# Kernel tuning notes

Measured on AMD Instinct MI355X. Metric: run time of the kernel, lower is better.

The kernel has to match this reference:

```python
import jax, jax.numpy as jnp
import numpy as np

N = 50000      # nodes
E = 800000     # edges (avg degree 16)
D_IN = 128     # input_dim
H = 64         # hidden_dim (== output_dim)
L = 3          # num_layers


def setup_inputs() -> dict:
    key = jax.random.key(0)
    ks = jax.random.split(key, 24)
    s = 0.05
    p = lambda k, shape: jax.random.normal(k, shape, dtype=jnp.float32) * s
    inp = {}
    inp["node_features"] = jax.random.normal(ks[0], (N, D_IN), dtype=jnp.float32)
    inp["edge_index"] = jax.random.randint(ks[1], (2, E), 0, N, dtype=jnp.int32)
    # pre_mlp: Linear-ReLU-Linear (setup_LRL_nn with hidden_sizes=[hidden_dim])
    inp["pre_w1"] = p(ks[2], (D_IN, H)); inp["pre_b1"] = jnp.zeros((H,), jnp.float32)
    inp["pre_w2"] = p(ks[3], (H, H));    inp["pre_b2"] = jnp.zeros((H,), jnp.float32)
    # learnable skip gates (initialized to ones as in the module)
    inp["skip"] = jnp.ones((L, L), jnp.float32)
    # SAGEConv layers: lin_l (on mean-aggregated neighbors, with bias) + lin_r (root)
    for i in range(L):
        din = H * (i + 1)
        inp[f"wl{i}"] = p(ks[4 + 3 * i], (din, H))
        inp[f"bl{i}"] = jnp.zeros((H,), jnp.float32)
        inp[f"wr{i}"] = p(ks[5 + 3 * i], (din, H))
    # post_mlp: 256->64, 64->64, 64->256, 256->64
    inp["post_w1"] = p(ks[14], (H * (L + 1), H)); inp["post_b1"] = jnp.zeros((H,), jnp.float32)
    inp["post_w2"] = p(ks[15], (H, H));           inp["post_b2"] = jnp.zeros((H,), jnp.float32)
    inp["post_w3"] = p(ks[16], (H, 256));         inp["post_b3"] = jnp.zeros((256,), jnp.float32)
    inp["post_w4"] = p(ks[17], (256, H));         inp["post_b4"] = jnp.zeros((H,), jnp.float32)
    return inp


def _sage(x, src, dst, inv_deg, wl, bl, wr):
    # PyG SAGEConv (mean aggr): lin_l(mean_{j->i} x_j) + lin_r(x_i)
    agg = jax.ops.segment_sum(x[src], dst, num_segments=N) * inv_deg  # [N, Din]
    return agg @ wl + bl + x @ wr


def reference(node_features, edge_index,
              pre_w1, pre_b1, pre_w2, pre_b2, skip,
              wl0, bl0, wr0, wl1, bl1, wr1, wl2, bl2, wr2,
              post_w1, post_b1, post_w2, post_b2, post_w3, post_b3, post_w4, post_b4):
    src, dst = edge_index[0], edge_index[1]
    deg = jax.ops.segment_sum(jnp.ones((E,), jnp.float32), dst, num_segments=N)
    inv_deg = (1.0 / jnp.maximum(deg, 1.0))[:, None]  # [N,1]

    # pre_mlp
    x = jax.nn.relu(node_features @ pre_w1 + pre_b1) @ pre_w2 + pre_b2  # [N,H]

    layers = [(wl0, bl0, wr0), (wl1, bl1, wr1), (wl2, bl2, wr2)]
    all_emb = [x]
    emb = x
    for i, (wl, bl, wr) in enumerate(layers):
        gates = jax.nn.sigmoid(skip[i, :i + 1])  # [i+1]
        curr = jnp.concatenate([all_emb[j] * gates[j] for j in range(i + 1)], axis=1)  # [N, H*(i+1)]
        h = jax.nn.relu(_sage(curr, src, dst, inv_deg, wl, bl, wr))  # [N,H]  (dropout p=0)
        emb = jnp.concatenate([emb, h], axis=1)
        all_emb.append(h)

    s = jnp.sum(emb, axis=-2)  # sums over all nodes -> [H*(L+1)] (faithful to source)
    h = jax.nn.leaky_relu(s @ post_w1 + post_b1, negative_slope=0.1)
    h = jax.nn.relu(h @ post_w2 + post_b2)
    h = jax.nn.relu(h @ post_w3 + post_b3)
    return h @ post_w4 + post_b4  # [H]
```

## Files before the change

### kernel.cpp

```cpp
#include <hip/hip_runtime.h>
#include <math.h>

#define NN 50000
#define NE 800000
#define NB 196

typedef float v4f __attribute__((ext_vector_type(4)));
typedef short v8s __attribute__((ext_vector_type(8)));

__device__ __forceinline__ unsigned short f2bf(float f) {
  unsigned u = __float_as_uint(f);
  u = u + 0x7FFFu + ((u >> 16) & 1u);
  return (unsigned short)(u >> 16);
}
__device__ __forceinline__ float bf2f(unsigned short h) {
  return __uint_as_float(((unsigned)h) << 16);
}


__global__ __launch_bounds__(256) void k_bhist(const int* __restrict__ dst,
                                               int* __restrict__ gbcnt) {
  __shared__ int lcnt[NB];
  int t = threadIdx.x;
  for (int i = t; i < NB; i += 256) lcnt[i] = 0;
  __syncthreads();
  int eb = blockIdx.x * 4096;
#pragma unroll
  for (int i = 0; i < 16; ++i) {
    int e = eb + i * 256 + t;
    if (e < NE) atomicAdd(&lcnt[dst[e] >> 8], 1);
  }
  __syncthreads();
  for (int i = t; i < NB; i += 256)
    if (lcnt[i]) atomicAdd(&gbcnt[i], lcnt[i]);
}

__global__ __launch_bounds__(256) void k_bscan(const int* __restrict__ gbcnt,
                                               int* __restrict__ boff,
                                               int* __restrict__ gcur,
                                               int* __restrict__ offs) {
  __shared__ int sd[256];
  int t = threadIdx.x;
  int v = (t < NB) ? gbcnt[t] : 0;
  sd[t] = v;
  __syncthreads();
  for (int o = 1; o < 256; o <<= 1) {
    int u = (t >= o) ? sd[t - o] : 0;
    __syncthreads();
    sd[t] += u;
    __syncthreads();
  }
  if (t < NB) { int x = sd[t] - v; boff[t] = x; gcur[t] = x; }
  if (t == NB - 1) boff[NB] = sd[t];
  if (t == 0) offs[NN] = NE;
}

__global__ __launch_bounds__(256) void k_bscatter(const int* __restrict__ src,
                                                  const int* __restrict__ dst,
                                                  int* __restrict__ gcur,
                                                  unsigned* __restrict__ ebuf) {
  __shared__ int cnt[NB];
  __shared__ int base[NB];
  int t = threadIdx.x;
  for (int i = t; i < NB; i += 256) cnt[i] = 0;
  __syncthreads();
  int eb = blockIdx.x * 4096;
  unsigned pk[16];
  int bk[16], lp[16];
#pragma unroll
  for (int i = 0; i < 16; ++i) {
    int e = eb + i * 256 + t;
    if (e < NE) {
      int d = dst[e];
      int b = d >> 8;
      pk[i] = ((unsigned)src[e] << 8) | (unsigned)(d & 255);
      bk[i] = b;
      lp[i] = atomicAdd(&cnt[b], 1);
    }
  }
  __syncthreads();
  for (int i = t; i < NB; i += 256)
    base[i] = cnt[i] ? atomicAdd(&gcur[i], cnt[i]) : 0;
  __syncthreads();
#pragma unroll
  for (int i = 0; i < 16; ++i) {
    int e = eb + i * 256 + t;
    if (e < NE) ebuf[base[bk[i]] + lp[i]] = pk[i];
  }
}

__global__ __launch_bounds__(256) void k_bbuild(const unsigned* __restrict__ ebuf,
                                                const int* __restrict__ boff,
                                                int* __restrict__ offs,
                                                float* __restrict__ invd,
                                                int* __restrict__ csr) {
  __shared__ int dcnt[256];
  __shared__ int cur[256];
  int t = threadIdx.x;
  int b = blockIdx.x;
  int node0 = b << 8;
  int es = boff[b], ee = boff[b + 1];
  dcnt[t] = 0;
  __syncthreads();
  for (int e = es + t; e < ee; e += 256) atomicAdd(&dcnt[ebuf[e] & 255], 1);
  __syncthreads();
  int v = dcnt[t];
  cur[t] = v;
  __syncthreads();
  for (int o = 1; o < 256; o <<= 1) {
    int u = (t >= o) ? cur[t - o] : 0;
    __syncthreads();
    cur[t] += u;
    __syncthreads();
  }
  int excl = cur[t] - v;
  int node = node0 + t;
  if (node < NN) {
    offs[node] = es + excl;
    invd[node] = 1.0f / fmaxf((float)v, 1.0f);
  }
  __syncthreads();
  cur[t] = es + excl;
  __syncthreads();
  for (int e = es + t; e < ee; e += 256) {
    unsigned pk = ebuf[e];
    int p = atomicAdd(&cur[pk & 255], 1);
    csr[p] = (int)(pk >> 8);
  }
}

__global__ __launch_bounds__(256) void k_aggregate(
    const unsigned short* __restrict__ feat,
    const int* __restrict__ offs, const int* __restrict__ csr,
    const float* __restrict__ invd,
    unsigned short* __restrict__ mean, int n) {
  int node = blockIdx.x * 4 + (threadIdx.x >> 6);
  int lane = threadIdx.x & 63;
  int nsub = lane >> 4;
  int cg   = lane & 15;
  if (node >= n) return;
  int s = offs[node], e = offs[node + 1];

  float a[8];
#pragma unroll
  for (int i = 0; i < 8; ++i) a[i] = 0.f;

  if (e > s) {
    int emax = e - 1;
    for (int p0 = s; p0 < e; p0 += 16) {
      int pa = p0 + nsub, pb = p0 + 4 + nsub, pc = p0 + 8 + nsub, pd = p0 + 12 + nsub;
      int ja = csr[pa < emax ? pa : emax];
      int jb = csr[pb < emax ? pb : emax];
      int jc = csr[pc < emax ? pc : emax];
      int jd = csr[pd < emax ? pd : emax];
      v8s va = *(const v8s*)(feat + (size_t)ja * 128 + cg * 8);
      v8s vb = *(const v8s*)(feat + (size_t)jb * 128 + cg * 8);
      v8s vc = *(const v8s*)(feat + (size_t)jc * 128 + cg * 8);
      v8s vd = *(const v8s*)(feat + (size_t)jd * 128 + cg * 8);
      if (pa < e) {
#pragma unroll
        for (int i = 0; i < 8; ++i) a[i] += bf2f((unsigned short)va[i]);
      }
      if (pb < e) {
#pragma unroll
        for (int i = 0; i < 8; ++i) a[i] += bf2f((unsigned short)vb[i]);
      }
      if (pc < e) {
#pragma unroll
        for (int i = 0; i < 8; ++i) a[i] += bf2f((unsigned short)vc[i]);
      }
      if (pd < e) {
#pragma unroll
        for (int i = 0; i < 8; ++i) a[i] += bf2f((unsigned short)vd[i]);
      }
    }
  }
#pragma unroll
  for (int i = 0; i < 8; ++i) {
    a[i] += __shfl_xor(a[i], 8, 64);
    a[i] += __shfl_xor(a[i], 16, 64);
    a[i] += __shfl_xor(a[i], 32, 64);
  }
  if (lane < 8) {
    float d = invd[node];
    v8s oh, ol;
#pragma unroll
    for (int i = 0; i < 8; ++i) {
      float m = a[i] * d;
      unsigned short h = f2bf(m);
      oh[i] = (short)h;
      ol[i] = (short)f2bf(m - bf2f(h));
    }
    *(v8s*)(mean + (size_t)node * 128 + lane * 8) = oh;
    *(v8s*)(mean + (size_t)node * 128 + 64 + lane * 8) = ol;
  }
}

struct WPrepArgs {
  const float* w[15];
  int gidx[15];
  const float* skip;
  unsigned short* wbuf;
};

__global__ __launch_bounds__(256) void k_wprep(WPrepArgs P) {
  int slot = blockIdx.x;
  int t = threadIdx.x;
  const float* w = P.w[slot];
  float gs = 1.0f;
  if (P.gidx[slot] >= 0) gs = 1.0f / (1.0f + __expf(-P.skip[P.gidx[slot]]));
  unsigned short* hi = P.wbuf + (size_t)slot * 8192;
  unsigned short* lo = hi + 4096;
#pragma unroll
  for (int half = 0; half < 2; ++half) {
    int p = t + 256 * half;
    int frag = p >> 6, lane = p & 63;
    int ks = frag >> 2, ct = frag & 3;
    int qd = lane >> 4, ln = lane & 15;
    v8s hv, lv;
#pragma unroll
    for (int j = 0; j < 8; ++j) {
      float f = w[(size_t)(ks * 32 + qd * 8 + j) * 64 + ct * 16 + ln] * gs;
      unsigned short h = f2bf(f);
      hv[j] = (short)h;
      lv[j] = (short)f2bf(f - bf2f(h));
    }
    *(v8s*)(hi + (size_t)p * 8) = hv;
    *(v8s*)(lo + (size_t)p * 8) = lv;
  }
}

struct LinArgs {
  const void* a[6];
  int isf32[6];
  int stride[6];
  int slot0;
  int nsrc;
  const float* bias;
  const unsigned short* wbuf;
  unsigned short* outp;
  float* colsum;
  int n;
  int relu;
};

__global__ __launch_bounds__(256) void k_linear(LinArgs A) {
  __shared__ float red[256];
  const int t    = threadIdx.x;
  const int lane = t & 63;
  const int wv   = t >> 6;
  const int qd   = lane >> 4;
  const int ln   = lane & 15;
  const int n0   = blockIdx.x * 64;

  v4f acc[4];
#pragma unroll
  for (int ct = 0; ct < 4; ++ct) acc[ct] = (v4f){0.f, 0.f, 0.f, 0.f};

  const int arow = n0 + wv * 16 + ln;
  const bool arv = arow < A.n;

  v8s rawh[2], rawl[2];
  float rawf[16];
  v8s curh[2], curl[2];
  auto loadA = [&](int s) {
    if (A.isf32[s]) {
      const float* a = (const float*)A.a[s];
      int st = A.stride[s];
      if (arv) {
#pragma unroll
        for (int ks = 0; ks < 2; ++ks) {
          const float* p = a + (size_t)arow * st + ks * 32 + qd * 8;
          float4 u0 = *(const float4*)(p);
          float4 u1 = *(const float4*)(p + 4);
          rawf[ks * 8 + 0] = u0.x; rawf[ks * 8 + 1] = u0.y;
          rawf[ks * 8 + 2] = u0.z; rawf[ks * 8 + 3] = u0.w;
          rawf[ks * 8 + 4] = u1.x; rawf[ks * 8 + 5] = u1.y;
          rawf[ks * 8 + 6] = u1.z; rawf[ks * 8 + 7] = u1.w;
        }
      } else {
#pragma unroll
        for (int j = 0; j < 16; ++j) rawf[j] = 0.f;
      }
    } else {
      const unsigned short* ph = (const unsigned short*)A.a[s] + (size_t)arow * 128;
      if (arv) {
#pragma unroll
        for (int ks = 0; ks < 2; ++ks) {
          rawh[ks] = *(const v8s*)(ph + ks * 32 + qd * 8);
          rawl[ks] = *(const v8s*)(ph + 64 + ks * 32 + qd * 8);
        }
      } else {
        v8s z;
#pragma unroll
        for (int j = 0; j < 8; ++j) z[j] = 0;
        rawh[0] = rawh[1] = rawl[0] = rawl[1] = z;
      }
    }
  };
  auto stageA = [&](int s) {
    if (A.isf32[s]) {
#pragma unroll
      for (int ks = 0; ks < 2; ++ks) {
        v8s hv, lv;
#pragma unroll
        for (int j = 0; j < 8; ++j) {
          float f = rawf[ks * 8 + j];
          unsigned short h = f2bf(f);
          hv[j] = (short)h;
          lv[j] = (short)f2bf(f - bf2f(h));
        }
        curh[ks] = hv; curl[ks] = lv;
      }
    } else {
#pragma unroll
      for (int ks = 0; ks < 2; ++ks) { curh[ks] = rawh[ks]; curl[ks] = rawl[ks]; }
    }
  };

  loadA(0);
  stageA(0);

  for (int s = 0; s < A.nsrc; ++s) {
    if (s + 1 < A.nsrc) loadA(s + 1);
    const unsigned short* wb = A.wbuf + (size_t)(A.slot0 + s) * 8192;
#pragma unroll
    for (int ks = 0; ks < 2; ++ks) {
#pragma unroll
      for (int ct = 0; ct < 4; ++ct) {
        const unsigned short* fp = wb + (size_t)((ks * 4 + ct) * 64 + lane) * 8;
        v8s bh = *(const v8s*)(fp);
        v8s bl = *(const v8s*)(fp + 4096);
        acc[ct] = __builtin_amdgcn_mfma_f32_16x16x32_bf16(curh[ks], bh, acc[ct], 0, 0, 0);
        acc[ct] = __builtin_amdgcn_mfma_f32_16x16x32_bf16(curl[ks], bh, acc[ct], 0, 0, 0);
        acc[ct] = __builtin_amdgcn_mfma_f32_16x16x32_bf16(curh[ks], bl, acc[ct], 0, 0, 0);
      }
    }
    if (s + 1 < A.nsrc) stageA(s + 1);
  }

  float bvals[4];
#pragma unroll
  for (int ct = 0; ct < 4; ++ct) bvals[ct] = A.bias[ct * 16 + ln];

  float cs[4] = {0.f, 0.f, 0.f, 0.f};
#pragma unroll
  for (int ct = 0; ct < 4; ++ct) {
#pragma unroll
    for (int r = 0; r < 4; ++r) {
      int node = n0 + wv * 16 + qd * 4 + r;
      float v = acc[ct][r] + bvals[ct];
      if (A.relu) v = fmaxf(v, 0.f);
      if (node < A.n) {
        unsigned short h = f2bf(v);
        A.outp[(size_t)node * 128 + ct * 16 + ln] = h;
        A.outp[(size_t)node * 128 + 64 + ct * 16 + ln] = f2bf(v - bf2f(h));
        cs[ct] += v;
      }
    }
  }
  if (A.colsum) {
#pragma unroll
    for (int ct = 0; ct < 4; ++ct) {
      float v = cs[ct];
      v += __shfl_xor(v, 16, 64);
      v += __shfl_xor(v, 32, 64);
      if (qd == 0) red[wv * 64 + ct * 16 + ln] = v;
    }
    __syncthreads();
    if (t < 64) {
      float ssum = red[t] + red[64 + t] + red[128 + t] + red[192 + t];
      atomicAdd(&A.colsum[t], ssum);
    }
  }
}

__global__ __launch_bounds__(256) void k_post(const float* __restrict__ s,
                                              const float* __restrict__ w1, const float* __restrict__ b1,
                                              const float* __restrict__ w2, const float* __restrict__ b2,
                                              const float* __restrict__ w3, const float* __restrict__ b3,
                                              const float* __restrict__ w4, const float* __restrict__ b4,
                                              float* __restrict__ outp) {
  __shared__ float sh[256], h1[64], h2[64], h3[256];
  int t = threadIdx.x;
  sh[t] = s[t];
  __syncthreads();
  if (t < 64) {
    float a = b1[t];
    for (int k = 0; k < 256; ++k) a += sh[k] * w1[k * 64 + t];
    h1[t] = (a >= 0.f) ? a : 0.1f * a;
  }
  __syncthreads();
  if (t < 64) {
    float a = b2[t];
    for (int k = 0; k < 64; ++k) a += h1[k] * w2[k * 64 + t];
    h2[t] = fmaxf(a, 0.f);
  }
  __syncthreads();
  {
    float a = b3[t];
    for (int k = 0; k < 64; ++k) a += h2[k] * w3[k * 256 + t];
    h3[t] = fmaxf(a, 0.f);
  }
  __syncthreads();
  if (t < 64) {
    float a = b4[t];
    for (int k = 0; k < 256; ++k) a += h3[k] * w4[k * 64 + t];
    outp[t] = a;
  }
}

extern "C" void kernel_launch(void* const* d_in, const int* in_sizes, int n_in,
                              void* d_out, int out_size, void* d_ws, size_t ws_size,
                              hipStream_t stream) {
  const float* nf     = (const float*)d_in[0];
  const int*   ei     = (const int*)d_in[1];
  const float* pre_w1 = (const float*)d_in[2];
  const float* pre_b1 = (const float*)d_in[3];
  const float* pre_w2 = (const float*)d_in[4];
  const float* pre_b2 = (const float*)d_in[5];
  const float* skip   = (const float*)d_in[6];
  const float* wl0 = (const float*)d_in[7],  *bl0 = (const float*)d_in[8],  *wr0 = (const float*)d_in[9];
  const float* wl1 = (const float*)d_in[10], *bl1 = (const float*)d_in[11], *wr1 = (const float*)d_in[12];
  const float* wl2 = (const float*)d_in[13], *bl2 = (const float*)d_in[14], *wr2 = (const float*)d_in[15];
  const float* pw1 = (const float*)d_in[16], *pb1 = (const float*)d_in[17];
  const float* pw2 = (const float*)d_in[18], *pb2 = (const float*)d_in[19];
  const float* pw3 = (const float*)d_in[20], *pb3 = (const float*)d_in[21];
  const float* pw4 = (const float*)d_in[22], *pb4 = (const float*)d_in[23];
  float* out = (float*)d_out;

  const int N = NN, E = NE;

  char* ws = (char*)d_ws;
  size_t pos = 0;
  auto alloc = [&](size_t bytes) {
    char* p = ws + pos;
    pos += (bytes + 255) & ~(size_t)255;
    return (void*)p;
  };
  int*      gbcnt = (int*)alloc((size_t)NB * 4);
  int*      boff  = (int*)alloc((size_t)(NB + 1) * 4);
  int*      gcur  = (int*)alloc((size_t)NB * 4);
  unsigned* ebuf  = (unsigned*)alloc((size_t)E * 4);
  int*      offs  = (int*)alloc((size_t)(N + 1) * 4);
  float*    invd  = (float*)alloc((size_t)N * 4);
  int*      csr   = (int*)alloc((size_t)E * 4);
  unsigned short* wbuf = (unsigned short*)alloc((size_t)15 * 8192 * 2);
  const size_t PB = (size_t)N * 128 * 2;
  unsigned short* x  = (unsigned short*)alloc(PB);
  unsigned short* h0 = (unsigned short*)alloc(PB);
  unsigned short* h1 = (unsigned short*)alloc(PB);
  unsigned short* h2 = (unsigned short*)alloc(PB);
  unsigned short* m0 = (unsigned short*)alloc(PB);
  unsigned short* m1 = (unsigned short*)alloc(PB);
  unsigned short* m2 = (unsigned short*)alloc(PB);
  unsigned short* t0 = m2;
  float* sv = (float*)alloc(256 * 4);

  hipMemsetAsync(gbcnt, 0, (size_t)NB * 4, stream);
  hipMemsetAsync(sv, 0, 256 * 4, stream);

  {
    WPrepArgs P;
    const float* wsrc[15] = {
      pre_w1, pre_w1 + 64 * 64,
      pre_w2,
      wl0, wr0,
      wl1, wl1 + 64 * 64, wr1, wr1 + 64 * 64,
      wl2, wl2 + 64 * 64, wl2 + 128 * 64,
      wr2, wr2 + 64 * 64, wr2 + 128 * 64
    };
    int gi[15] = {-1, -1, -1, 0, 0, 3, 4, 3, 4, 6, 7, 8, 6, 7, 8};
    for (int i = 0; i < 15; ++i) { P.w[i] = wsrc[i]; P.gidx[i] = gi[i]; }
    P.skip = skip; P.wbuf = wbuf;
    k_wprep<<<15, 256, 0, stream>>>(P);
  }

  const int* e_src = ei;
  const int* e_dst = ei + E;
  const int EGRID = (E + 4095) / 4096;
  k_bhist<<<EGRID, 256, 0, stream>>>(e_dst, gbcnt);
  k_bscan<<<1, 256, 0, stream>>>(gbcnt, boff, gcur, offs);
  k_bscatter<<<EGRID, 256, 0, stream>>>(e_src, e_dst, gcur, ebuf);
  k_bbuild<<<NB, 256, 0, stream>>>(ebuf, boff, offs, invd, csr);

  const int LGRID = (N + 63) / 64;
  auto lin = [&](int nsrc, int slot0,
                 const void* a0, int f0, int s0,
                 const void* a1, int f1, int s1,
                 const void* a2, int f2, int s2,
                 const void* a3, int f3, int s3,
                 const void* a4, int f4, int s4,
                 const void* a5, int f5, int s5,
                 const float* bias, unsigned short* op, float* colsum, int relu) {
    LinArgs A;
    A.a[0] = a0; A.a[1] = a1; A.a[2] = a2; A.a[3] = a3; A.a[4] = a4; A.a[5] = a5;
    A.isf32[0] = f0; A.isf32[1] = f1; A.isf32[2] = f2; A.isf32[3] = f3; A.isf32[4] = f4; A.isf32[5] = f5;
    A.stride[0] = s0; A.stride[1] = s1; A.stride[2] = s2; A.stride[3] = s3; A.stride[4] = s4; A.stride[5] = s5;
    A.slot0 = slot0; A.nsrc = nsrc; A.bias = bias; A.wbuf = wbuf;
    A.outp = op; A.colsum = colsum;
    A.n = N; A.relu = relu;
    k_linear<<<LGRID, 256, 0, stream>>>(A);
  };

  lin(2, 0, nf, 1, 128, nf + 64, 1, 128,
      nullptr, 0, 0, nullptr, 0, 0, nullptr, 0, 0, nullptr, 0, 0,
      pre_b1, t0, nullptr, 1);
  lin(1, 2, t0, 0, 0,
      nullptr, 0, 0, nullptr, 0, 0, nullptr, 0, 0, nullptr, 0, 0, nullptr, 0, 0,
      pre_b2, x, sv, 0);

  k_aggregate<<<(N + 3) / 4, 256, 0, stream>>>(x, offs, csr, invd, m0, N);
  lin(2, 3, m0, 0, 0, x, 0, 0,
      nullptr, 0, 0, nullptr, 0, 0, nullptr, 0, 0, nullptr, 0, 0,
      bl0, h0, sv + 64, 1);

  k_aggregate<<<(N + 3) / 4, 256, 0, stream>>>(h0, offs, csr, invd, m1, N);
  lin(4, 5, m0, 0, 0, m1, 0, 0, x, 0, 0, h0, 0, 0,
      nullptr, 0, 0, nullptr, 0, 0,
      bl1, h1, sv + 128, 1);

  k_aggregate<<<(N + 3) / 4, 256, 0, stream>>>(h1, offs, csr, invd, m2, N);
  lin(6, 9, m0, 0, 0, m1, 0, 0, m2, 0, 0, x, 0, 0, h0, 0, 0, h1, 0, 0,
      bl2, h2, sv + 192, 1);

  k_post<<<1, 256, 0, stream>>>(sv, pw1, pb1, pw2, pb2, pw3, pb3, pw4, pb4, out);
}
```

Baseline: 407.7 us.

## Compute later-layer partial products early and carry fp32 partials across layers

Each SAGE layer's concatenated input is split into per-source blocks. Every block is now loaded once, in the first linear kernel that sees it, and multiplied there against the weight slices for all later layers. The partial sums are kept in fp32 buffers (p1, p2) and fed into the next layer's accumulators. This removes the re-reading and re-staging of m0, x, m1 and h0 in layers 1 and 2, which previously reloaded up to six 64-wide sources. In exchange it adds fp32 partial-sum reads and writes of N×64 floats per carried set, and raises register pressure in the NSET=3 kernel instantiation.

```diff
diff --git a/kernel.cpp b/kernel.cpp
--- a/kernel.cpp
+++ b/kernel.cpp
@@ -231,19 +231,22 @@
 }
 
 struct LinArgs {
-  const void* a[6];
-  int isf32[6];
-  int stride[6];
-  int slot0;
+  const void* a[2];
+  int isf32[2];
+  int stride[2];
   int nsrc;
-  const float* bias;
+  int wslot[2][3];
+  const float* pin[3];
+  const float* bias[3];
+  unsigned short* outp[3];
+  float* pout[3];
+  int relu[3];
+  float* colsum;
   const unsigned short* wbuf;
-  unsigned short* outp;
-  float* colsum;
   int n;
-  int relu;
 };
 
+template <int NSET>
 __global__ __launch_bounds__(256) void k_linear(LinArgs A) {
   __shared__ float red[256];
   const int t    = threadIdx.x;
@@ -253,12 +256,28 @@
   const int ln   = lane & 15;
   const int n0   = blockIdx.x * 64;
 
-  v4f acc[4];
-#pragma unroll
-  for (int ct = 0; ct < 4; ++ct) acc[ct] = (v4f){0.f, 0.f, 0.f, 0.f};
+  v4f acc[NSET][4];
+#pragma unroll
+  for (int c = 0; c < NSET; ++c)
+#pragma unroll
+    for (int ct = 0; ct < 4; ++ct) acc[c][ct] = (v4f){0.f, 0.f, 0.f, 0.f};
 
   const int arow = n0 + wv * 16 + ln;
   const bool arv = arow < A.n;
+
+#pragma unroll
+  for (int c = 0; c < NSET; ++c) {
+    if (A.pin[c]) {
+      const float* p = A.pin[c];
+#pragma unroll
+      for (int ct = 0; ct < 4; ++ct)
+#pragma unroll
+        for (int r = 0; r < 4; ++r) {
+          int node = n0 + wv * 16 + qd * 4 + r;
+          if (node < A.n) acc[c][ct][r] = p[(size_t)node * 64 + ct * 16 + ln];
+        }
+    }
+  }
 
   v8s rawh[2], rawl[2];
   float rawf[16];
@@ -323,42 +342,50 @@
 
   for (int s = 0; s < A.nsrc; ++s) {
     if (s + 1 < A.nsrc) loadA(s + 1);
-    const unsigned short* wb = A.wbuf + (size_t)(A.slot0 + s) * 8192;
-#pragma unroll
-    for (int ks = 0; ks < 2; ++ks) {
-#pragma unroll
-      for (int ct = 0; ct < 4; ++ct) {
-        const unsigned short* fp = wb + (size_t)((ks * 4 + ct) * 64 + lane) * 8;
-        v8s bh = *(const v8s*)(fp);
-        v8s bl = *(const v8s*)(fp + 4096);
-        acc[ct] = __builtin_amdgcn_mfma_f32_16x16x32_bf16(curh[ks], bh, acc[ct], 0, 0, 0);
-        acc[ct] = __builtin_amdgcn_mfma_f32_16x16x32_bf16(curl[ks], bh, acc[ct], 0, 0, 0);
-        acc[ct] = __builtin_amdgcn_mfma_f32_16x16x32_bf16(curh[ks], bl, acc[ct], 0, 0, 0);
+#pragma unroll
+    for (int c = 0; c < NSET; ++c) {
+      const unsigned short* wb = A.wbuf + (size_t)A.wslot[s][c] * 8192;
+#pragma unroll
+      for (int ks = 0; ks < 2; ++ks) {
+#pragma unroll
+        for (int ct = 0; ct < 4; ++ct) {
+          const unsigned short* fp = wb + (size_t)((ks * 4 + ct) * 64 + lane) * 8;
+          v8s bh = *(const v8s*)(fp);
+          v8s bl = *(const v8s*)(fp + 4096);
+          acc[c][ct] = __builtin_amdgcn_mfma_f32_16x16x32_bf16(curh[ks], bh, acc[c][ct], 0, 0, 0);
+          acc[c][ct] = __builtin_amdgcn_mfma_f32_16x16x32_bf16(curl[ks], bh, acc[c][ct], 0, 0, 0);
+          acc[c][ct] = __builtin_amdgcn_mfma_f32_16x16x32_bf16(curh[ks], bl, acc[c][ct], 0, 0, 0);
+        }
       }
     }
     if (s + 1 < A.nsrc) stageA(s + 1);
   }
 
-  float bvals[4];
-#pragma unroll
-  for (int ct = 0; ct < 4; ++ct) bvals[ct] = A.bias[ct * 16 + ln];
-
   float cs[4] = {0.f, 0.f, 0.f, 0.f};
 #pragma unroll
-  for (int ct = 0; ct < 4; ++ct) {
-#pragma unroll
-    for (int r = 0; r < 4; ++r) {
-      int node = n0 + wv * 16 + qd * 4 + r;
-      float v = acc[ct][r] + bvals[ct];
-      if (A.relu) v = fmaxf(v, 0.f);
-      if (node < A.n) {
-        unsigned short h = f2bf(v);
-        A.outp[(size_t)node * 128 + ct * 16 + ln] = h;
-        A.outp[(size_t)node * 128 + 64 + ct * 16 + ln] = f2bf(v - bf2f(h));
-        cs[ct] += v;
-      }
-    }
-  }
+  for (int c = 0; c < NSET; ++c) {
+    float bvals[4];
+#pragma unroll
+    for (int ct = 0; ct < 4; ++ct) bvals[ct] = A.bias[c] ? A.bias[c][ct * 16 + ln] : 0.f;
+#pragma unroll
+    for (int ct = 0; ct < 4; ++ct) {
+#pragma unroll
+      for (int r = 0; r < 4; ++r) {
+        int node = n0 + wv * 16 + qd * 4 + r;
+        if (node >= A.n) continue;
+        float v = acc[c][ct][r] + bvals[ct];
+        if (A.relu[c]) v = fmaxf(v, 0.f);
+        if (A.outp[c]) {
+          unsigned short h = f2bf(v);
+          A.outp[c][(size_t)node * 128 + ct * 16 + ln] = h;
+          A.outp[c][(size_t)node * 128 + 64 + ct * 16 + ln] = f2bf(v - bf2f(h));
+          if (c == 0) cs[ct] += v;
+        }
+        if (A.pout[c]) A.pout[c][(size_t)node * 64 + ct * 16 + ln] = v;
+      }
+    }
+  }
+
   if (A.colsum) {
 #pragma unroll
     for (int ct = 0; ct < 4; ++ct) {
@@ -455,6 +482,8 @@
   unsigned short* m1 = (unsigned short*)alloc(PB);
   unsigned short* m2 = (unsigned short*)alloc(PB);
   unsigned short* t0 = m2;
+  float* p1 = (float*)alloc((size_t)N * 64 * 4);
+  float* p2 = (float*)alloc((size_t)N * 64 * 4);
   float* sv = (float*)alloc(256 * 4);
 
   hipMemsetAsync(gbcnt, 0, (size_t)NB * 4, stream);
@@ -485,44 +514,77 @@
   k_bbuild<<<NB, 256, 0, stream>>>(ebuf, boff, offs, invd, csr);
 
   const int LGRID = (N + 63) / 64;
-  auto lin = [&](int nsrc, int slot0,
-                 const void* a0, int f0, int s0,
-                 const void* a1, int f1, int s1,
-                 const void* a2, int f2, int s2,
-                 const void* a3, int f3, int s3,
-                 const void* a4, int f4, int s4,
-                 const void* a5, int f5, int s5,
-                 const float* bias, unsigned short* op, float* colsum, int relu) {
-    LinArgs A;
-    A.a[0] = a0; A.a[1] = a1; A.a[2] = a2; A.a[3] = a3; A.a[4] = a4; A.a[5] = a5;
-    A.isf32[0] = f0; A.isf32[1] = f1; A.isf32[2] = f2; A.isf32[3] = f3; A.isf32[4] = f4; A.isf32[5] = f5;
-    A.stride[0] = s0; A.stride[1] = s1; A.stride[2] = s2; A.stride[3] = s3; A.stride[4] = s4; A.stride[5] = s5;
-    A.slot0 = slot0; A.nsrc = nsrc; A.bias = bias; A.wbuf = wbuf;
-    A.outp = op; A.colsum = colsum;
-    A.n = N; A.relu = relu;
-    k_linear<<<LGRID, 256, 0, stream>>>(A);
+
+  auto zero3p = [](LinArgs& A) {
+    for (int c = 0; c < 3; ++c) {
+      A.pin[c] = nullptr; A.bias[c] = nullptr; A.outp[c] = nullptr;
+      A.pout[c] = nullptr; A.relu[c] = 0;
+      A.wslot[0][c] = 0; A.wslot[1][c] = 0;
+    }
+    A.colsum = nullptr;
   };
 
-  lin(2, 0, nf, 1, 128, nf + 64, 1, 128,
-      nullptr, 0, 0, nullptr, 0, 0, nullptr, 0, 0, nullptr, 0, 0,
-      pre_b1, t0, nullptr, 1);
-  lin(1, 2, t0, 0, 0,
-      nullptr, 0, 0, nullptr, 0, 0, nullptr, 0, 0, nullptr, 0, 0, nullptr, 0, 0,
-      pre_b2, x, sv, 0);
+  {
+    LinArgs A; zero3p(A);
+    A.a[0] = nf;      A.isf32[0] = 1; A.stride[0] = 128;
+    A.a[1] = nf + 64; A.isf32[1] = 1; A.stride[1] = 128;
+    A.nsrc = 2;
+    A.wslot[0][0] = 0; A.wslot[1][0] = 1;
+    A.bias[0] = pre_b1; A.outp[0] = t0; A.relu[0] = 1;
+    A.wbuf = wbuf; A.n = N;
+    k_linear<1><<<LGRID, 256, 0, stream>>>(A);
+  }
+  {
+    LinArgs A; zero3p(A);
+    A.a[0] = t0; A.isf32[0] = 0; A.stride[0] = 0;
+    A.nsrc = 1;
+    A.wslot[0][0] = 2;
+    A.bias[0] = pre_b2; A.outp[0] = x; A.relu[0] = 0; A.colsum = sv;
+    A.wbuf = wbuf; A.n = N;
+    k_linear<1><<<LGRID, 256, 0, stream>>>(A);
+  }
 
   k_aggregate<<<(N + 3) / 4, 256, 0, stream>>>(x, offs, csr, invd, m0, N);
-  lin(2, 3, m0, 0, 0, x, 0, 0,
-      nullptr, 0, 0, nullptr, 0, 0, nullptr, 0, 0, nullptr, 0, 0,
-      bl0, h0, sv + 64, 1);
+  {
+    LinArgs A; zero3p(A);
+    A.a[0] = m0; A.isf32[0] = 0; A.stride[0] = 0;
+    A.a[1] = x;  A.isf32[1] = 0; A.stride[1] = 0;
+    A.nsrc = 2;
+    A.wslot[0][0] = 3;  A.wslot[1][0] = 4;
+    A.wslot[0][1] = 5;  A.wslot[1][1] = 7;
+    A.wslot[0][2] = 9;  A.wslot[1][2] = 12;
+    A.bias[0] = bl0; A.outp[0] = h0; A.relu[0] = 1; A.colsum = sv + 64;
+    A.pout[1] = p1;
+    A.pout[2] = p2;
+    A.wbuf = wbuf; A.n = N;
+    k_linear<3><<<LGRID, 256, 0, stream>>>(A);
+  }
 
   k_aggregate<<<(N + 3) / 4, 256, 0, stream>>>(h0, offs, csr, invd, m1, N);
-  lin(4, 5, m0, 0, 0, m1, 0, 0, x, 0, 0, h0, 0, 0,
-      nullptr, 0, 0, nullptr, 0, 0,
-      bl1, h1, sv + 128, 1);
+  {
+    LinArgs A; zero3p(A);
+    A.a[0] = m1; A.isf32[0] = 0; A.stride[0] = 0;
+    A.a[1] = h0; A.isf32[1] = 0; A.stride[1] = 0;
+    A.nsrc = 2;
+    A.wslot[0][0] = 6;  A.wslot[1][0] = 8;
+    A.wslot[0][1] = 10; A.wslot[1][1] = 13;
+    A.pin[0] = p1; A.bias[0] = bl1; A.outp[0] = h1; A.relu[0] = 1; A.colsum = sv + 128;
+    A.pin[1] = p2; A.pout[1] = p2;
+    A.wbuf = wbuf; A.n = N;
+    k_linear<2><<<LGRID, 256, 0, stream>>>(A);
+  }
 
   k_aggregate<<<(N + 3) / 4, 256, 0, stream>>>(h1, offs, csr, invd, m2, N);
-  lin(6, 9, m0, 0, 0, m1, 0, 0, m2, 0, 0, x, 0, 0, h0, 0, 0, h1, 0, 0,
-      bl2, h2, sv + 192, 1);
+  {
+    LinArgs A; zero3p(A);
+    A.a[0] = m2; A.isf32[0] = 0; A.stride[0] = 0;
+    A.a[1] = h1; A.isf32[1] = 0; A.stride[1] = 0;
+    A.nsrc = 2;
+    A.wslot[0][0] = 11; A.wslot[1][0] = 14;
+    A.pin[0] = p2; A.bias[0] = bl2; A.outp[0] = h2; A.relu[0] = 1; A.colsum = sv + 192;
+    A.wbuf = wbuf; A.n = N;
+    k_linear<1><<<LGRID, 256, 0, stream>>>(A);
+  }
 
   k_post<<<1, 256, 0, stream>>>(sv, pw1, pb1, pw2, pb2, pw3, pb3, pw4, pb4, out);
 }
```

After: 442.1 us. 1.08x slower.

## Fuse neighbor aggregation into layer GEMM kernels and fuse pre-MLP layers

Applied to the files above, without the earlier changes.

Neighbor mean aggregation now runs inside each layer kernel: a 1024-thread block gathers its 64 rows into shared memory and feeds them straight into the MFMA linear stage. This removes the separate aggregate launches and the global write and re-read of the last mean buffer. The two pre-MLP linears are fused through shared memory, which eliminates the intermediate global tensor. Work is split so each wave computes one 16-column tile rather than all four, trading per-wave reuse for more waves. The gather and GEMM phases are now serialized within a block behind a barrier, which may reduce latency hiding.

```diff
diff --git a/kernel.cpp b/kernel.cpp
--- a/kernel.cpp
+++ b/kernel.cpp
@@ -129,73 +129,6 @@
   }
 }
 
-__global__ __launch_bounds__(256) void k_aggregate(
-    const unsigned short* __restrict__ feat,
-    const int* __restrict__ offs, const int* __restrict__ csr,
-    const float* __restrict__ invd,
-    unsigned short* __restrict__ mean, int n) {
-  int node = blockIdx.x * 4 + (threadIdx.x >> 6);
-  int lane = threadIdx.x & 63;
-  int nsub = lane >> 4;
-  int cg   = lane & 15;
-  if (node >= n) return;
-  int s = offs[node], e = offs[node + 1];
-
-  float a[8];
-#pragma unroll
-  for (int i = 0; i < 8; ++i) a[i] = 0.f;
-
-  if (e > s) {
-    int emax = e - 1;
-    for (int p0 = s; p0 < e; p0 += 16) {
-      int pa = p0 + nsub, pb = p0 + 4 + nsub, pc = p0 + 8 + nsub, pd = p0 + 12 + nsub;
-      int ja = csr[pa < emax ? pa : emax];
-      int jb = csr[pb < emax ? pb : emax];
-      int jc = csr[pc < emax ? pc : emax];
-      int jd = csr[pd < emax ? pd : emax];
-      v8s va = *(const v8s*)(feat + (size_t)ja * 128 + cg * 8);
-      v8s vb = *(const v8s*)(feat + (size_t)jb * 128 + cg * 8);
-      v8s vc = *(const v8s*)(feat + (size_t)jc * 128 + cg * 8);
-      v8s vd = *(const v8s*)(feat + (size_t)jd * 128 + cg * 8);
-      if (pa < e) {
-#pragma unroll
-        for (int i = 0; i < 8; ++i) a[i] += bf2f((unsigned short)va[i]);
-      }
-      if (pb < e) {
-#pragma unroll
-        for (int i = 0; i < 8; ++i) a[i] += bf2f((unsigned short)vb[i]);
-      }
-      if (pc < e) {
-#pragma unroll
-        for (int i = 0; i < 8; ++i) a[i] += bf2f((unsigned short)vc[i]);
-      }
-      if (pd < e) {
-#pragma unroll
-        for (int i = 0; i < 8; ++i) a[i] += bf2f((unsigned short)vd[i]);
-      }
-    }
-  }
-#pragma unroll
-  for (int i = 0; i < 8; ++i) {
-    a[i] += __shfl_xor(a[i], 8, 64);
-    a[i] += __shfl_xor(a[i], 16, 64);
-    a[i] += __shfl_xor(a[i], 32, 64);
-  }
-  if (lane < 8) {
-    float d = invd[node];
-    v8s oh, ol;
-#pragma unroll
-    for (int i = 0; i < 8; ++i) {
-      float m = a[i] * d;
-      unsigned short h = f2bf(m);
-      oh[i] = (short)h;
-      ol[i] = (short)f2bf(m - bf2f(h));
-    }
-    *(v8s*)(mean + (size_t)node * 128 + lane * 8) = oh;
-    *(v8s*)(mean + (size_t)node * 128 + 64 + lane * 8) = ol;
-  }
-}
-
 struct WPrepArgs {
   const float* w[15];
   int gidx[15];
@@ -230,149 +163,265 @@
   }
 }
 
-struct LinArgs {
-  const void* a[6];
-  int isf32[6];
-  int stride[6];
-  int slot0;
+struct PreArgs {
+  const float* nf;
+  const float* b1;
+  const float* b2;
+  const unsigned short* wbuf;
+  unsigned short* outx;
+  float* colsum;
+  int n;
+};
+
+__global__ __launch_bounds__(1024) void k_pre(PreArgs A) {
+  __shared__ unsigned short sm[64 * 136];
+  const int t    = threadIdx.x;
+  const int wv   = t >> 6;
+  const int lane = t & 63;
+  const int rb   = wv >> 2, cs = wv & 3;
+  const int qd   = lane >> 4, ln = lane & 15;
+  const int n0   = blockIdx.x * 64;
+  const int arow = n0 + rb * 16 + ln;
+  const bool arv = arow < A.n;
+
+  v4f acc1 = (v4f){0.f, 0.f, 0.f, 0.f};
+#pragma unroll
+  for (int src = 0; src < 2; ++src) {
+    v8s ah[2], al[2];
+#pragma unroll
+    for (int ks = 0; ks < 2; ++ks) {
+      float f[8];
+      if (arv) {
+        const float* p = A.nf + (size_t)arow * 128 + src * 64 + ks * 32 + qd * 8;
+        float4 u0 = *(const float4*)(p);
+        float4 u1 = *(const float4*)(p + 4);
+        f[0] = u0.x; f[1] = u0.y; f[2] = u0.z; f[3] = u0.w;
+        f[4] = u1.x; f[5] = u1.y; f[6] = u1.z; f[7] = u1.w;
+      } else {
+#pragma unroll
+        for (int j = 0; j < 8; ++j) f[j] = 0.f;
+      }
+      v8s hv, lv;
+#pragma unroll
+      for (int j = 0; j < 8; ++j) {
+        unsigned short h = f2bf(f[j]);
+        hv[j] = (short)h;
+        lv[j] = (short)f2bf(f[j] - bf2f(h));
+      }
+      ah[ks] = hv; al[ks] = lv;
+    }
+    const unsigned short* wb = A.wbuf + (size_t)src * 8192;
+#pragma unroll
+    for (int ks = 0; ks < 2; ++ks) {
+      const unsigned short* fp = wb + (size_t)((ks * 4 + cs) * 64 + lane) * 8;
+      v8s bh = *(const v8s*)(fp);
+      v8s bl = *(const v8s*)(fp + 4096);
+      acc1 = __builtin_amdgcn_mfma_f32_16x16x32_bf16(ah[ks], bh, acc1, 0, 0, 0);
+      acc1 = __builtin_amdgcn_mfma_f32_16x16x32_bf16(al[ks], bh, acc1, 0, 0, 0);
+      acc1 = __builtin_amdgcn_mfma_f32_16x16x32_bf16(ah[ks], bl, acc1, 0, 0, 0);
+    }
+  }
+  {
+    float bv = A.b1[cs * 16 + ln];
+#pragma unroll
+    for (int r = 0; r < 4; ++r) {
+      int row = rb * 16 + qd * 4 + r;
+      float v = fmaxf(acc1[r] + bv, 0.f);
+      unsigned short h = f2bf(v);
+      sm[row * 136 + cs * 16 + ln] = h;
+      sm[row * 136 + 64 + cs * 16 + ln] = f2bf(v - bf2f(h));
+    }
+  }
+  __syncthreads();
+
+  v4f acc2 = (v4f){0.f, 0.f, 0.f, 0.f};
+  {
+    const unsigned short* p = sm + (size_t)(rb * 16 + ln) * 136 + qd * 8;
+    v8s ah0 = *(const v8s*)(p);
+    v8s al0 = *(const v8s*)(p + 64);
+    v8s ah1 = *(const v8s*)(p + 32);
+    v8s al1 = *(const v8s*)(p + 96);
+    const unsigned short* wb = A.wbuf + (size_t)2 * 8192;
+#pragma unroll
+    for (int ks = 0; ks < 2; ++ks) {
+      const unsigned short* fp = wb + (size_t)((ks * 4 + cs) * 64 + lane) * 8;
+      v8s bh = *(const v8s*)(fp);
+      v8s bl = *(const v8s*)(fp + 4096);
+      v8s ah = ks ? ah1 : ah0, al = ks ? al1 : al0;
+      acc2 = __builtin_amdgcn_mfma_f32_16x16x32_bf16(ah, bh, acc2, 0, 0, 0);
+      acc2 = __builtin_amdgcn_mfma_f32_16x16x32_bf16(al, bh, acc2, 0, 0, 0);
+      acc2 = __builtin_amdgcn_mfma_f32_16x16x32_bf16(ah, bl, acc2, 0, 0, 0);
+    }
+  }
+  float cv = 0.f;
+  float bv = A.b2[cs * 16 + ln];
+#pragma unroll
+  for (int r = 0; r < 4; ++r) {
+    int node = n0 + rb * 16 + qd * 4 + r;
+    if (node >= A.n) continue;
+    float v = acc2[r] + bv;
+    unsigned short h = f2bf(v);
+    A.outx[(size_t)node * 128 + cs * 16 + ln] = h;
+    A.outx[(size_t)node * 128 + 64 + cs * 16 + ln] = f2bf(v - bf2f(h));
+    cv += v;
+  }
+  cv += __shfl_xor(cv, 16, 64);
+  cv += __shfl_xor(cv, 32, 64);
+  if (qd == 0) atomicAdd(&A.colsum[cs * 16 + ln], cv);
+}
+
+struct LayerArgs {
+  const unsigned short* gfeat;
+  const int* offs; const int* csr; const float* invd;
+  unsigned short* mean_out;
+  const unsigned short* asrc[6];
+  int wslot[6];
   int nsrc;
   const float* bias;
   const unsigned short* wbuf;
   unsigned short* outp;
   float* colsum;
   int n;
-  int relu;
 };
 
-__global__ __launch_bounds__(256) void k_linear(LinArgs A) {
-  __shared__ float red[256];
+__global__ __launch_bounds__(1024) void k_layer(LayerArgs A) {
+  __shared__ unsigned short sm[64 * 136];
   const int t    = threadIdx.x;
+  const int wv   = t >> 6;
   const int lane = t & 63;
-  const int wv   = t >> 6;
-  const int qd   = lane >> 4;
-  const int ln   = lane & 15;
   const int n0   = blockIdx.x * 64;
 
-  v4f acc[4];
-#pragma unroll
-  for (int ct = 0; ct < 4; ++ct) acc[ct] = (v4f){0.f, 0.f, 0.f, 0.f};
-
-  const int arow = n0 + wv * 16 + ln;
+  {
+    const int nsub = lane >> 4, cg = lane & 15;
+    for (int g = 0; g < 4; ++g) {
+      const int row = wv * 4 + g;
+      const int node = n0 + row;
+      float a[8];
+#pragma unroll
+      for (int i = 0; i < 8; ++i) a[i] = 0.f;
+      if (node < A.n) {
+        int s = A.offs[node], e = A.offs[node + 1];
+        if (e > s) {
+          int emax = e - 1;
+          for (int p0 = s; p0 < e; p0 += 16) {
+            int pa = p0 + nsub, pb = p0 + 4 + nsub, pc = p0 + 8 + nsub, pd = p0 + 12 + nsub;
+            int ja = A.csr[pa < emax ? pa : emax];
+            int jb = A.csr[pb < emax ? pb : emax];
+            int jc = A.csr[pc < emax ? pc : emax];
+            int jd = A.csr[pd < emax ? pd : emax];
+            v8s va = *(const v8s*)(A.gfeat + (size_t)ja * 128 + cg * 8);
+            v8s vb = *(const v8s*)(A.gfeat + (size_t)jb * 128 + cg * 8);
+            v8s vc = *(const v8s*)(A.gfeat + (size_t)jc * 128 + cg * 8);
+            v8s vd = *(const v8s*)(A.gfeat + (size_t)jd * 128 + cg * 8);
+            if (pa < e) {
+#pragma unroll
+              for (int i = 0; i < 8; ++i) a[i] += bf2f((unsigned short)va[i]);
+            }
+            if (pb < e) {
+#pragma unroll
+              for (int i = 0; i < 8; ++i) a[i] += bf2f((unsigned short)vb[i]);
+            }
+            if (pc < e) {
+#pragma unroll
+              for (int i = 0; i < 8; ++i) a[i] += bf2f((unsigned short)vc[i]);
+            }
+            if (pd < e) {
+#pragma unroll
+              for (int i = 0; i < 8; ++i) a[i] += bf2f((unsigned short)vd[i]);
+            }
+          }
+        }
+      }
+#pragma unroll
+      for (int i = 0; i < 8; ++i) {
+        a[i] += __shfl_xor(a[i], 8, 64);
+        a[i] += __shfl_xor(a[i], 16, 64);
+        a[i] += __shfl_xor(a[i], 32, 64);
+      }
+      if (lane < 8) {
+        float d = (node < A.n) ? A.invd[node] : 0.f;
+        v8s oh, ol;
+#pragma unroll
+        for (int i = 0; i < 8; ++i) {
+          float m = a[i] * d;
+          unsigned short h = f2bf(m);
+          oh[i] = (short)h;
+          ol[i] = (short)f2bf(m - bf2f(h));
+        }
+        *(v8s*)(sm + (size_t)row * 136 + lane * 8) = oh;
+        *(v8s*)(sm + (size_t)row * 136 + 64 + lane * 8) = ol;
+        if (A.mean_out && node < A.n) {
+          *(v8s*)(A.mean_out + (size_t)node * 128 + lane * 8) = oh;
+          *(v8s*)(A.mean_out + (size_t)node * 128 + 64 + lane * 8) = ol;
+        }
+      }
+    }
+  }
+  __syncthreads();
+
+  const int rb = wv >> 2, cs = wv & 3;
+  const int qd = lane >> 4, ln = lane & 15;
+  v4f acc = (v4f){0.f, 0.f, 0.f, 0.f};
+  const int arow = n0 + rb * 16 + ln;
   const bool arv = arow < A.n;
 
-  v8s rawh[2], rawl[2];
-  float rawf[16];
-  v8s curh[2], curl[2];
-  auto loadA = [&](int s) {
-    if (A.isf32[s]) {
-      const float* a = (const float*)A.a[s];
-      int st = A.stride[s];
-      if (arv) {
-#pragma unroll
-        for (int ks = 0; ks < 2; ++ks) {
-          const float* p = a + (size_t)arow * st + ks * 32 + qd * 8;
-          float4 u0 = *(const float4*)(p);
-          float4 u1 = *(const float4*)(p + 4);
-          rawf[ks * 8 + 0] = u0.x; rawf[ks * 8 + 1] = u0.y;
-          rawf[ks * 8 + 2] = u0.z; rawf[ks * 8 + 3] = u0.w;
-          rawf[ks * 8 + 4] = u1.x; rawf[ks * 8 + 5] = u1.y;
-          rawf[ks * 8 + 6] = u1.z; rawf[ks * 8 + 7] = u1.w;
-        }
-      } else {
-#pragma unroll
-        for (int j = 0; j < 16; ++j) rawf[j] = 0.f;
+  v8s curh[2], curl[2], rawh[2], rawl[2];
+  {
+    const unsigned short* p = sm + (size_t)(rb * 16 + ln) * 136 + qd * 8;
+    curh[0] = *(const v8s*)(p);
+    curl[0] = *(const v8s*)(p + 64);
+    curh[1] = *(const v8s*)(p + 32);
+    curl[1] = *(const v8s*)(p + 96);
+  }
+  auto loadG = [&](int s) {
+    if (arv) {
+      const unsigned short* ph = A.asrc[s] + (size_t)arow * 128;
+#pragma unroll
+      for (int ks = 0; ks < 2; ++ks) {
+        rawh[ks] = *(const v8s*)(ph + ks * 32 + qd * 8);
+        rawl[ks] = *(const v8s*)(ph + 64 + ks * 32 + qd * 8);
       }
     } else {
-      const unsigned short* ph = (const unsigned short*)A.a[s] + (size_t)arow * 128;
-      if (arv) {
-#pragma unroll
-        for (int ks = 0; ks < 2; ++ks) {
-          rawh[ks] = *(const v8s*)(ph + ks * 32 + qd * 8);
-          rawl[ks] = *(const v8s*)(ph + 64 + ks * 32 + qd * 8);
-        }
-      } else {
-        v8s z;
-#pragma unroll
-        for (int j = 0; j < 8; ++j) z[j] = 0;
-        rawh[0] = rawh[1] = rawl[0] = rawl[1] = z;
-      }
+      v8s z;
+#pragma unroll
+      for (int j = 0; j < 8; ++j) z[j] = 0;
+      rawh[0] = rawh[1] = rawl[0] = rawl[1] = z;
     }
   };
-  auto stageA = [&](int s) {
-    if (A.isf32[s]) {
-#pragma unroll
-      for (int ks = 0; ks < 2; ++ks) {
-        v8s hv, lv;
-#pragma unroll
-        for (int j = 0; j < 8; ++j) {
-          float f = rawf[ks * 8 + j];
-          unsigned short h = f2bf(f);
-          hv[j] = (short)h;
-          lv[j] = (short)f2bf(f - bf2f(h));
-        }
-        curh[ks] = hv; curl[ks] = lv;
-      }
-    } else {
-#pragma unroll
-      for (int ks = 0; ks < 2; ++ks) { curh[ks] = rawh[ks]; curl[ks] = rawl[ks]; }
-    }
-  };
-
-  loadA(0);
-  stageA(0);
 
   for (int s = 0; s < A.nsrc; ++s) {
-    if (s + 1 < A.nsrc) loadA(s + 1);
-    const unsigned short* wb = A.wbuf + (size_t)(A.slot0 + s) * 8192;
+    if (s + 1 < A.nsrc) loadG(s + 1);
+    const unsigned short* wb = A.wbuf + (size_t)A.wslot[s] * 8192;
 #pragma unroll
     for (int ks = 0; ks < 2; ++ks) {
-#pragma unroll
-      for (int ct = 0; ct < 4; ++ct) {
-        const unsigned short* fp = wb + (size_t)((ks * 4 + ct) * 64 + lane) * 8;
-        v8s bh = *(const v8s*)(fp);
-        v8s bl = *(const v8s*)(fp + 4096);
-        acc[ct] = __builtin_amdgcn_mfma_f32_16x16x32_bf16(curh[ks], bh, acc[ct], 0, 0, 0);
-        acc[ct] = __builtin_amdgcn_mfma_f32_16x16x32_bf16(curl[ks], bh, acc[ct], 0, 0, 0);
-        acc[ct] = __builtin_amdgcn_mfma_f32_16x16x32_bf16(curh[ks], bl, acc[ct], 0, 0, 0);
-      }
-    }
-    if (s + 1 < A.nsrc) stageA(s + 1);
-  }
-
-  float bvals[4];
-#pragma unroll
-  for (int ct = 0; ct < 4; ++ct) bvals[ct] = A.bias[ct * 16 + ln];
-
-  float cs[4] = {0.f, 0.f, 0.f, 0.f};
-#pragma unroll
-  for (int ct = 0; ct < 4; ++ct) {
-#pragma unroll
-    for (int r = 0; r < 4; ++r) {
-      int node = n0 + wv * 16 + qd * 4 + r;
-      float v = acc[ct][r] + bvals[ct];
-      if (A.relu) v = fmaxf(v, 0.f);
-      if (node < A.n) {
-        unsigned short h = f2bf(v);
-        A.outp[(size_t)node * 128 + ct * 16 + ln] = h;
-        A.outp[(size_t)node * 128 + 64 + ct * 16 + ln] = f2bf(v - bf2f(h));
-        cs[ct] += v;
-      }
-    }
-  }
-  if (A.colsum) {
-#pragma unroll
-    for (int ct = 0; ct < 4; ++ct) {
-      float v = cs[ct];
-      v += __shfl_xor(v, 16, 64);
-      v += __shfl_xor(v, 32, 64);
-      if (qd == 0) red[wv * 64 + ct * 16 + ln] = v;
-    }
-    __syncthreads();
-    if (t < 64) {
-      float ssum = red[t] + red[64 + t] + red[128 + t] + red[192 + t];
-      atomicAdd(&A.colsum[t], ssum);
-    }
-  }
+      const unsigned short* fp = wb + (size_t)((ks * 4 + cs) * 64 + lane) * 8;
+      v8s bh = *(const v8s*)(fp);
+      v8s bl = *(const v8s*)(fp + 4096);
+      acc = __builtin_amdgcn_mfma_f32_16x16x32_bf16(curh[ks], bh, acc, 0, 0, 0);
+      acc = __builtin_amdgcn_mfma_f32_16x16x32_bf16(curl[ks], bh, acc, 0, 0, 0);
+      acc = __builtin_amdgcn_mfma_f32_16x16x32_bf16(curh[ks], bl, acc, 0, 0, 0);
+    }
+    if (s + 1 < A.nsrc) {
+      curh[0] = rawh[0]; curh[1] = rawh[1];
+      curl[0] = rawl[0]; curl[1] = rawl[1];
+    }
+  }
+
+  float cv = 0.f;
+  float bv = A.bias[cs * 16 + ln];
+#pragma unroll
+  for (int r = 0; r < 4; ++r) {
+    int node = n0 + rb * 16 + qd * 4 + r;
+    if (node >= A.n) continue;
+    float v = fmaxf(acc[r] + bv, 0.f);
+    unsigned short h = f2bf(v);
+    A.outp[(size_t)node * 128 + cs * 16 + ln] = h;
+    A.outp[(size_t)node * 128 + 64 + cs * 16 + ln] = f2bf(v - bf2f(h));
+    cv += v;
+  }
+  cv += __shfl_xor(cv, 16, 64);
+  cv += __shfl_xor(cv, 32, 64);
+  if (qd == 0) atomicAdd(&A.colsum[cs * 16 + ln], cv);
 }
 
 __global__ __launch_bounds__(256) void k_post(const float* __restrict__ s,
@@ -453,8 +502,6 @@
   unsigned short* h2 = (unsigned short*)alloc(PB);
   unsigned short* m0 = (unsigned short*)alloc(PB);
   unsigned short* m1 = (unsigned short*)alloc(PB);
-  unsigned short* m2 = (unsigned short*)alloc(PB);
-  unsigned short* t0 = m2;
   float* sv = (float*)alloc(256 * 4);
 
   hipMemsetAsync(gbcnt, 0, (size_t)NB * 4, stream);
@@ -485,44 +532,39 @@
   k_bbuild<<<NB, 256, 0, stream>>>(ebuf, boff, offs, invd, csr);
 
   const int LGRID = (N + 63) / 64;
-  auto lin = [&](int nsrc, int slot0,
-                 const void* a0, int f0, int s0,
-                 const void* a1, int f1, int s1,
-                 const void* a2, int f2, int s2,
-                 const void* a3, int f3, int s3,
-                 const void* a4, int f4, int s4,
-                 const void* a5, int f5, int s5,
-                 const float* bias, unsigned short* op, float* colsum, int relu) {
-    LinArgs A;
-    A.a[0] = a0; A.a[1] = a1; A.a[2] = a2; A.a[3] = a3; A.a[4] = a4; A.a[5] = a5;
-    A.isf32[0] = f0; A.isf32[1] = f1; A.isf32[2] = f2; A.isf32[3] = f3; A.isf32[4] = f4; A.isf32[5] = f5;
-    A.stride[0] = s0; A.stride[1] = s1; A.stride[2] = s2; A.stride[3] = s3; A.stride[4] = s4; A.stride[5] = s5;
-    A.slot0 = slot0; A.nsrc = nsrc; A.bias = bias; A.wbuf = wbuf;
-    A.outp = op; A.colsum = colsum;
-    A.n = N; A.relu = relu;
-    k_linear<<<LGRID, 256, 0, stream>>>(A);
+
+  {
+    PreArgs P;
+    P.nf = nf; P.b1 = pre_b1; P.b2 = pre_b2;
+    P.wbuf = wbuf; P.outx = x; P.colsum = sv; P.n = N;
+    k_pre<<<LGRID, 1024, 0, stream>>>(P);
+  }
+
+  auto layer = [&](const unsigned short* gfeat, unsigned short* mean_out,
+                   int nsrc,
+                   const unsigned short* a1, const unsigned short* a2,
+                   const unsigned short* a3, const unsigned short* a4,
+                   const unsigned short* a5,
+                   int s0, int s1, int s2, int s3, int s4, int s5,
+                   const float* bias, unsigned short* outp, float* colsum) {
+    LayerArgs A;
+    A.gfeat = gfeat; A.offs = offs; A.csr = csr; A.invd = invd;
+    A.mean_out = mean_out;
+    A.asrc[0] = nullptr; A.asrc[1] = a1; A.asrc[2] = a2;
+    A.asrc[3] = a3; A.asrc[4] = a4; A.asrc[5] = a5;
+    A.wslot[0] = s0; A.wslot[1] = s1; A.wslot[2] = s2;
+    A.wslot[3] = s3; A.wslot[4] = s4; A.wslot[5] = s5;
+    A.nsrc = nsrc; A.bias = bias; A.wbuf = wbuf;
+    A.outp = outp; A.colsum = colsum; A.n = N;
+    k_layer<<<LGRID, 1024, 0, stream>>>(A);
   };
 
-  lin(2, 0, nf, 1, 128, nf + 64, 1, 128,
-      nullptr, 0, 0, nullptr, 0, 0, nullptr, 0, 0, nullptr, 0, 0,
-      pre_b1, t0, nullptr, 1);
-  lin(1, 2, t0, 0, 0,
-      nullptr, 0, 0, nullptr, 0, 0, nullptr, 0, 0, nullptr, 0, 0, nullptr, 0, 0,
-      pre_b2, x, sv, 0);
-
-  k_aggregate<<<(N + 3) / 4, 256, 0, stream>>>(x, offs, csr, invd, m0, N);
-  lin(2, 3, m0, 0, 0, x, 0, 0,
-      nullptr, 0, 0, nullptr, 0, 0, nullptr, 0, 0, nullptr, 0, 0,
-      bl0, h0, sv + 64, 1);
-
-  k_aggregate<<<(N + 3) / 4, 256, 0, stream>>>(h0, offs, csr, invd, m1, N);
-  lin(4, 5, m0, 0, 0, m1, 0, 0, x, 0, 0, h0, 0, 0,
-      nullptr, 0, 0, nullptr, 0, 0,
-      bl1, h1, sv + 128, 1);
-
-  k_aggregate<<<(N + 3) / 4, 256, 0, stream>>>(h1, offs, csr, invd, m2, N);
-  lin(6, 9, m0, 0, 0, m1, 0, 0, m2, 0, 0, x, 0, 0, h0, 0, 0, h1, 0, 0,
-      bl2, h2, sv + 192, 1);
+  layer(x, m0, 2, x, nullptr, nullptr, nullptr, nullptr,
+        3, 4, 0, 0, 0, 0, bl0, h0, sv + 64);
+  layer(h0, m1, 4, m0, x, h0, nullptr, nullptr,
+        6, 5, 7, 8, 0, 0, bl1, h1, sv + 128);
+  layer(h1, nullptr, 6, m0, m1, x, h0, h1,
+        11, 9, 10, 12, 13, 14, bl2, h2, sv + 192);
 
   k_post<<<1, 256, 0, stream>>>(sv, pw1, pb1, pw2, pb2, pw3, pb3, pw4, pb4, out);
 }
```

Result: slower. 675.7 us (+65.7%).
